# Performance work log

Measured on AMD Instinct MI355X. Metric: run time of the kernel, lower is better.

## Reference

```python
import jax, jax.numpy as jnp
import numpy as np

D_MODEL = 2048
NUM_HEADS = 16
D_FF = 8192
EPS = 1e-5


def setup_inputs() -> dict:
    key = jax.random.key(0)
    ks = jax.random.split(key, 9)
    s = 0.02
    return {
        "x": jax.random.normal(ks[0], (2, 2048, D_MODEL), dtype=jnp.float32),
        "wq": jax.random.normal(ks[1], (D_MODEL, D_MODEL), dtype=jnp.float32) * s,
        "wk": jax.random.normal(ks[2], (D_MODEL, D_MODEL), dtype=jnp.float32) * s,
        "wv": jax.random.normal(ks[3], (D_MODEL, D_MODEL), dtype=jnp.float32) * s,
        "wo": jax.random.normal(ks[4], (D_MODEL, D_MODEL), dtype=jnp.float32) * s,
        "w1": jax.random.normal(ks[5], (D_FF, D_MODEL), dtype=jnp.float32) * s,
        "w2": jax.random.normal(ks[6], (D_MODEL, D_FF), dtype=jnp.float32) * s,
        "g1": jnp.ones((D_MODEL,), dtype=jnp.float32),
        "g2": jnp.ones((D_MODEL,), dtype=jnp.float32),
    }


def rmsnorm(a, g):
    rms = jnp.sqrt(jnp.sum(a * a, axis=-1, keepdims=True) / a.shape[-1] + EPS)
    return a / rms * g


def attention(xn, wq, wk, wv, wo):
    B, S, D = xn.shape
    H, dk = NUM_HEADS, D // NUM_HEADS
    # Linear weights are (out, in); y = x @ W^T
    q = (xn @ wq.T).reshape(B, S, H, dk).transpose(0, 2, 1, 3)  # bhsd
    k = (xn @ wk.T).reshape(B, S, H, dk).transpose(0, 2, 1, 3)
    v = (xn @ wv.T).reshape(B, S, H, dk).transpose(0, 2, 1, 3)
    scores = jnp.einsum("bhqd,bhkd->bhqk", q, k) * (dk ** -0.5)
    causal = jnp.triu(jnp.ones((S, S), dtype=bool), k=1)
    scores = jnp.where(causal, -jnp.inf, scores)
    probs = jax.nn.softmax(scores, axis=-1)
    out = jnp.einsum("bhqk,bhkd->bhqd", probs, v)
    out = out.transpose(0, 2, 1, 3).reshape(B, S, D)
    return out @ wo.T


def reference(x, wq, wk, wv, wo, w1, w2, g1, g2):
    x = x + attention(rmsnorm(x, g1), wq, wk, wv, wo)
    h = jax.nn.gelu(rmsnorm(x, g2) @ w1.T, approximate=False)
    x = x + h @ w2.T
    return x
```

## Files before the change

### kernel.cpp

```cpp
#include <hip/hip_runtime.h>
#include <hip/hip_bf16.h>
#include <math.h>

#define D_MODEL 2048
#define SEQ     2048
#define BATCH   2
#define NHEAD   16
#define DK      128
#define DFF     8192
#define MROWS   (BATCH*SEQ)

typedef short short8 __attribute__((ext_vector_type(8)));
typedef float f32x4  __attribute__((ext_vector_type(4)));

__device__ __forceinline__ short f2bf(float f) {
  union { __hip_bfloat16 b; short s; } u;
  u.b = __float2bfloat16(f);
  return u.s;
}

__device__ __forceinline__ void gload_lds16(const void* g, void* l) {
  __builtin_amdgcn_global_load_lds(
      (const __attribute__((address_space(1))) unsigned int*)g,
      (__attribute__((address_space(3))) unsigned int*)l, 16, 0, 0);
}

__global__ __launch_bounds__(256) void rmsnorm_k(const float* __restrict__ x,
                                                 const float* __restrict__ g,
                                                 short* __restrict__ o) {
  const int row = blockIdx.x;
  const int t = threadIdx.x;
  const float4* xr = (const float4*)(x + (size_t)row * D_MODEL);
  const float4* gr = (const float4*)g;
  float4 v0 = xr[2*t], v1 = xr[2*t+1];
  float s = v0.x*v0.x + v0.y*v0.y + v0.z*v0.z + v0.w*v0.w
          + v1.x*v1.x + v1.y*v1.y + v1.z*v1.z + v1.w*v1.w;
  #pragma unroll
  for (int off = 1; off < 64; off <<= 1) s += __shfl_xor(s, off);
  __shared__ float red[4];
  if ((t & 63) == 0) red[t >> 6] = s;
  __syncthreads();
  float tot = red[0] + red[1] + red[2] + red[3];
  float inv = rsqrtf(tot * (1.0f / D_MODEL) + 1e-5f);
  float4 g0 = gr[2*t], g1v = gr[2*t+1];
  short8 ov;
  ov[0] = f2bf(v0.x * inv * g0.x);
  ov[1] = f2bf(v0.y * inv * g0.y);
  ov[2] = f2bf(v0.z * inv * g0.z);
  ov[3] = f2bf(v0.w * inv * g0.w);
  ov[4] = f2bf(v1.x * inv * g1v.x);
  ov[5] = f2bf(v1.y * inv * g1v.y);
  ov[6] = f2bf(v1.z * inv * g1v.z);
  ov[7] = f2bf(v1.w * inv * g1v.w);
  *((short8*)(o + (size_t)row * D_MODEL) + t) = ov;
}

__global__ __launch_bounds__(256) void f2b_k(const float* __restrict__ src,
                                             short* __restrict__ dst, int n8) {
  int i = blockIdx.x * 256 + threadIdx.x;
  if (i >= n8) return;
  const float4* s4 = (const float4*)src + 2 * (size_t)i;
  float4 a = s4[0], b = s4[1];
  short8 o = { f2bf(a.x), f2bf(a.y), f2bf(a.z), f2bf(a.w),
               f2bf(b.x), f2bf(b.y), f2bf(b.z), f2bf(b.w) };
  *((short8*)dst + i) = o;
}

template<int EPI>
__global__ __launch_bounds__(256) void gemm_fast(const short* __restrict__ A,
                                                 const short* __restrict__ B,
                                                 void* Cv,
                                                 const float* __restrict__ resid,
                                                 int M, int N, int K) {
  __shared__ __align__(16) short As[128 * 64];
  __shared__ __align__(16) short Bs[128 * 64];
  const int t = threadIdx.x;
  const int m0 = blockIdx.x * 128, n0 = blockIdx.y * 128;
  const int wave = t >> 6, lane = t & 63, lr = lane & 15, lg = lane >> 4;
  const int wr = (wave >> 1) * 64, wc = (wave & 1) * 64;

  f32x4 acc[4][4];
  const f32x4 z4 = {0.f, 0.f, 0.f, 0.f};
  #pragma unroll
  for (int m = 0; m < 4; ++m)
    #pragma unroll
    for (int n = 0; n < 4; ++n) acc[m][n] = z4;

  const int srow = t >> 3;
  const int scol = (t & 7) * 8;

  for (int k0 = 0; k0 < K; k0 += 64) {
    #pragma unroll
    for (int i = 0; i < 4; ++i) {
      int r = srow + 32 * i;
      gload_lds16(A + (size_t)(m0 + r) * K + k0 + scol, &As[r * 64 + scol]);
      gload_lds16(B + (size_t)(n0 + r) * K + k0 + scol, &Bs[r * 64 + scol]);
    }
    __syncthreads();
    #pragma unroll
    for (int kk = 0; kk < 64; kk += 32) {
      short8 af[4], bfr[4];
      #pragma unroll
      for (int m = 0; m < 4; ++m) af[m]  = *(const short8*)&As[(wr + m*16 + lr) * 64 + kk + lg*8];
      #pragma unroll
      for (int n = 0; n < 4; ++n) bfr[n] = *(const short8*)&Bs[(wc + n*16 + lr) * 64 + kk + lg*8];
      #pragma unroll
      for (int m = 0; m < 4; ++m)
        #pragma unroll
        for (int n = 0; n < 4; ++n)
          acc[m][n] = __builtin_amdgcn_mfma_f32_16x16x32_bf16(af[m], bfr[n], acc[m][n], 0, 0, 0);
    }
    __syncthreads();
  }

  #pragma unroll
  for (int m = 0; m < 4; ++m)
    #pragma unroll
    for (int n = 0; n < 4; ++n)
      #pragma unroll
      for (int r = 0; r < 4; ++r) {
        int row = m0 + wr + m*16 + lg*4 + r;
        int col = n0 + wc + n*16 + lr;
        size_t idx = (size_t)row * N + col;
        float vv = acc[m][n][r];
        if (EPI == 0) {
          ((short*)Cv)[idx] = f2bf(vv);
        } else if (EPI == 1) {
          float gl = 0.5f * vv * (1.0f + erff(vv * 0.70710678118654752f));
          ((short*)Cv)[idx] = f2bf(gl);
        } else {
          ((float*)Cv)[idx] = vv + resid[idx];
        }
      }
}

__global__ __launch_bounds__(256) void vtrans(const short* __restrict__ QKV,
                                              short* __restrict__ VT) {
  const int st = blockIdx.x;
  const int bh = blockIdx.y;
  const int b = bh >> 4, h = bh & 15;
  const int t = threadIdx.x;
  __shared__ __align__(16) short T[64 * 128];
  const short* Vsrc = QKV + ((size_t)b * SEQ) * 6144 + 2 * D_MODEL + h * DK;
  {
    int r = t >> 4, c = (t & 15) * 8;
    #pragma unroll
    for (int i = 0; i < 4; ++i) {
      int rr = r + 16 * i;
      uint4 vv = *(const uint4*)(Vsrc + (size_t)(st * 64 + rr) * 6144 + c);
      *(uint4*)&T[rr * 128 + (c ^ (((rr >> 3) & 7) << 3))] = vv;
    }
  }
  __syncthreads();
  short* dst = VT + ((size_t)bh * DK) * SEQ + st * 64;
  {
    int c2 = (t & 7) * 8;
    #pragma unroll
    for (int i = 0; i < 4; ++i) {
      int d = (t >> 3) + 32 * i;
      short8 ov;
      #pragma unroll
      for (int j = 0; j < 8; ++j)
        ov[j] = T[(c2 + j) * 128 + (d ^ ((((c2 + j) >> 3) & 7) << 3))];
      *(short8*)(dst + (size_t)d * SEQ + c2) = ov;
    }
  }
}

__global__ __launch_bounds__(512, 2) void attn3(const short* __restrict__ QKV,
                                                const short* __restrict__ VT,
                                                short* __restrict__ O) {
  const float SC = 0.12751743f;
  const int a = blockIdx.x, bh = blockIdx.y;
  const int b = bh >> 4, h = bh & 15;
  const int t = threadIdx.x, w = t >> 6, lane = t & 63, lr = lane & 15, lg = lane >> 4;
  const short* Qp = QKV + ((size_t)b * SEQ) * 6144 + h * DK;
  const short* Kp = Qp + D_MODEL;
  const short* Vp = VT + ((size_t)bh * DK) * SEQ;
  __shared__ __align__(16) short Ks[2][64 * 128];
  __shared__ __align__(16) short Vs[2][128 * 64];
  __shared__ __align__(16) short Ps[8][16][72];

  const int krr = t >> 4, kcc = (t & 15) * 8;
  const int vdd = t >> 3, vcc = (t & 7) * 8;
  const f32x4 z4 = {0.f, 0.f, 0.f, 0.f};

  for (int sub = 0; sub < 2; ++sub) {
    const int ts = sub ? (15 - a) : a;
    const int nt = 2 * ts + 2;
    const int qrow0 = ts * 128 + w * 16;

    short8 qf[4];
    #pragma unroll
    for (int ki = 0; ki < 4; ++ki)
      qf[ki] = *(const short8*)(Qp + (size_t)(qrow0 + lr) * 6144 + ki * 32 + lg * 8);

    f32x4 acc[8];
    #pragma unroll
    for (int nd = 0; nd < 8; ++nd) acc[nd] = z4;
    float mrow[4], lsum[4];
    #pragma unroll
    for (int r = 0; r < 4; ++r) { mrow[r] = -INFINITY; lsum[r] = 0.f; }

    uint4 krg[2], vrg[2];
    #pragma unroll
    for (int i = 0; i < 2; ++i) {
      krg[i] = *(const uint4*)(Kp + (size_t)(krr + 32 * i) * 6144 + kcc);
      vrg[i] = *(const uint4*)(Vp + (size_t)(vdd + 64 * i) * SEQ + vcc);
    }
    __syncthreads();
    #pragma unroll
    for (int i = 0; i < 2; ++i) {
      int r = krr + 32 * i;
      *(uint4*)&Ks[0][(r * 128 + kcc) ^ ((r & 7) << 3)] = krg[i];
      int d = vdd + 64 * i;
      *(uint4*)&Vs[0][(d * 64 + vcc) ^ ((d & 7) << 3)] = vrg[i];
    }
    __syncthreads();

    int cur = 0;
    for (int tt = 0; tt < nt; ++tt) {
      const bool pre = (tt + 1 < nt);
      if (pre) {
        #pragma unroll
        for (int i = 0; i < 2; ++i) {
          krg[i] = *(const uint4*)(Kp + (size_t)((tt + 1) * 64 + krr + 32 * i) * 6144 + kcc);
          vrg[i] = *(const uint4*)(Vp + (size_t)(vdd + 64 * i) * SEQ + (tt + 1) * 64 + vcc);
        }
      }

      f32x4 sf[4] = {z4, z4, z4, z4};
      #pragma unroll
      for (int ki = 0; ki < 4; ++ki) {
        #pragma unroll
        for (int nk = 0; nk < 4; ++nk) {
          int rr = nk * 16 + lr;
          short8 kf = *(const short8*)&Ks[cur][(rr * 128 + ki * 32 + lg * 8) ^ ((rr & 7) << 3)];
          sf[nk] = __builtin_amdgcn_mfma_f32_16x16x32_bf16(qf[ki], kf, sf[nk], 0, 0, 0);
        }
      }

      const bool diag = (tt * 64 + 63 > qrow0);
      #pragma unroll
      for (int r = 0; r < 4; ++r) {
        int qg = qrow0 + lg * 4 + r;
        float s0 = sf[0][r] * SC, s1 = sf[1][r] * SC, s2 = sf[2][r] * SC, s3 = sf[3][r] * SC;
        if (diag) {
          int c0 = tt * 64 + lr;
          s0 = (c0      <= qg) ? s0 : -3.0e38f;
          s1 = (c0 + 16 <= qg) ? s1 : -3.0e38f;
          s2 = (c0 + 32 <= qg) ? s2 : -3.0e38f;
          s3 = (c0 + 48 <= qg) ? s3 : -3.0e38f;
        }
        float mx = fmaxf(fmaxf(s0, s1), fmaxf(s2, s3));
        mx = fmaxf(mx, __shfl_xor(mx, 1));
        mx = fmaxf(mx, __shfl_xor(mx, 2));
        mx = fmaxf(mx, __shfl_xor(mx, 4));
        mx = fmaxf(mx, __shfl_xor(mx, 8));
        float mnew = fmaxf(mrow[r], mx);
        float alpha = exp2f(mrow[r] - mnew);
        mrow[r] = mnew;
        float p0 = exp2f(s0 - mnew), p1 = exp2f(s1 - mnew),
              p2 = exp2f(s2 - mnew), p3 = exp2f(s3 - mnew);
        lsum[r] = lsum[r] * alpha + ((p0 + p1) + (p2 + p3));
        #pragma unroll
        for (int nd = 0; nd < 8; ++nd) acc[nd][r] *= alpha;
        short* pr = &Ps[w][lg * 4 + r][0];
        pr[lr]      = f2bf(p0);
        pr[16 + lr] = f2bf(p1);
        pr[32 + lr] = f2bf(p2);
        pr[48 + lr] = f2bf(p3);
      }
      asm volatile("s_waitcnt lgkmcnt(0)" ::: "memory");
      __builtin_amdgcn_sched_barrier(0);

      short8 pf0 = *(const short8*)&Ps[w][lr][lg * 8];
      short8 pf1 = *(const short8*)&Ps[w][lr][32 + lg * 8];
      #pragma unroll
      for (int nd = 0; nd < 8; ++nd) {
        int rr = nd * 16 + lr;
        short8 vf0 = *(const short8*)&Vs[cur][(rr * 64 + lg * 8) ^ ((rr & 7) << 3)];
        short8 vf1 = *(const short8*)&Vs[cur][(rr * 64 + 32 + lg * 8) ^ ((rr & 7) << 3)];
        acc[nd] = __builtin_amdgcn_mfma_f32_16x16x32_bf16(pf0, vf0, acc[nd], 0, 0, 0);
        acc[nd] = __builtin_amdgcn_mfma_f32_16x16x32_bf16(pf1, vf1, acc[nd], 0, 0, 0);
      }
      __syncthreads();
      if (pre) {
        #pragma unroll
        for (int i = 0; i < 2; ++i) {
          int r = krr + 32 * i;
          *(uint4*)&Ks[cur ^ 1][(r * 128 + kcc) ^ ((r & 7) << 3)] = krg[i];
          int d = vdd + 64 * i;
          *(uint4*)&Vs[cur ^ 1][(d * 64 + vcc) ^ ((d & 7) << 3)] = vrg[i];
        }
      }
      __syncthreads();
      cur ^= 1;
    }

    float inv[4];
    #pragma unroll
    for (int r = 0; r < 4; ++r) {
      float ls = lsum[r];
      ls += __shfl_xor(ls, 1);
      ls += __shfl_xor(ls, 2);
      ls += __shfl_xor(ls, 4);
      ls += __shfl_xor(ls, 8);
      inv[r] = 1.0f / ls;
    }
    #pragma unroll
    for (int nd = 0; nd < 8; ++nd)
      #pragma unroll
      for (int r = 0; r < 4; ++r) {
        int row = qrow0 + lg * 4 + r;
        O[(size_t)(b * SEQ + row) * D_MODEL + h * DK + nd * 16 + lr] = f2bf(acc[nd][r] * inv[r]);
      }
  }
}

template<int EPI>
__global__ __launch_bounds__(256) void gemm_bt(const short* __restrict__ A,
                                               const float* __restrict__ B,
                                               void* Cv,
                                               const float* resid,
                                               int M, int N, int K) {
  __shared__ __align__(16) short As[128][72];
  __shared__ __align__(16) short Bs[128][72];
  const int t = threadIdx.x;
  const int m0 = blockIdx.x * 128, n0 = blockIdx.y * 128;
  const int wave = t >> 6, lane = t & 63, lr = lane & 15, lg = lane >> 4;
  const int wr = (wave >> 1) * 64, wc = (wave & 1) * 64;

  f32x4 acc[4][4];
  const f32x4 z4 = {0.f, 0.f, 0.f, 0.f};
  #pragma unroll
  for (int m = 0; m < 4; ++m)
    #pragma unroll
    for (int n = 0; n < 4; ++n) acc[m][n] = z4;

  int ar[4], ac[4];
  #pragma unroll
  for (int i = 0; i < 4; ++i) { int u = t + 256*i; ar[i] = u >> 3; ac[i] = (u & 7) * 8; }

  for (int k0 = 0; k0 < K; k0 += 64) {
    #pragma unroll
    for (int i = 0; i < 4; ++i) {
      uint4 va = *(const uint4*)(A + (size_t)(m0 + ar[i]) * K + k0 + ac[i]);
      *(uint4*)&As[ar[i]][ac[i]] = va;
    }
    #pragma unroll
    for (int i = 0; i < 4; ++i) {
      const float4* bp = (const float4*)(B + (size_t)(n0 + ar[i]) * K + k0 + ac[i]);
      float4 b0 = bp[0], b1 = bp[1];
      short8 pb = { f2bf(b0.x), f2bf(b0.y), f2bf(b0.z), f2bf(b0.w),
                    f2bf(b1.x), f2bf(b1.y), f2bf(b1.z), f2bf(b1.w) };
      *(short8*)&Bs[ar[i]][ac[i]] = pb;
    }
    __syncthreads();
    #pragma unroll
    for (int kk = 0; kk < 64; kk += 32) {
      short8 af[4], bfr[4];
      #pragma unroll
      for (int m = 0; m < 4; ++m) af[m]  = *(const short8*)&As[wr + m*16 + lr][kk + lg*8];
      #pragma unroll
      for (int n = 0; n < 4; ++n) bfr[n] = *(const short8*)&Bs[wc + n*16 + lr][kk + lg*8];
      #pragma unroll
      for (int m = 0; m < 4; ++m)
        #pragma unroll
        for (int n = 0; n < 4; ++n)
          acc[m][n] = __builtin_amdgcn_mfma_f32_16x16x32_bf16(af[m], bfr[n], acc[m][n], 0, 0, 0);
    }
    __syncthreads();
  }

  #pragma unroll
  for (int m = 0; m < 4; ++m)
    #pragma unroll
    for (int n = 0; n < 4; ++n)
      #pragma unroll
      for (int r = 0; r < 4; ++r) {
        int row = m0 + wr + m*16 + lg*4 + r;
        int col = n0 + wc + n*16 + lr;
        size_t idx = (size_t)row * N + col;
        float vv = acc[m][n][r];
        if (EPI == 0) {
          ((short*)Cv)[idx] = f2bf(vv);
        } else if (EPI == 1) {
          float gl = 0.5f * vv * (1.0f + erff(vv * 0.70710678118654752f));
          ((short*)Cv)[idx] = f2bf(gl);
        } else {
          ((float*)Cv)[idx] = vv + resid[idx];
        }
      }
}

__global__ __launch_bounds__(256) void attn_k(const short* __restrict__ Q,
                                              const short* __restrict__ K,
                                              const short* __restrict__ V,
                                              short* __restrict__ O) {
  const float scale = 0.08838834764831845f;
  const int qt = blockIdx.x;
  const int bh = blockIdx.y;
  const int b = bh >> 4, h = bh & 15;
  const size_t base = ((size_t)b * SEQ) * D_MODEL + (size_t)h * DK;
  const int t = threadIdx.x, wave = t >> 6, lane = t & 63, lr = lane & 15, lg = lane >> 4;

  __shared__ __align__(16) short Ks[32][136];
  __shared__ __align__(16) short Vt[128][40];
  __shared__ __align__(16) short Ps[4][32][40];

  const int qrow0 = qt * 128 + wave * 32;
  short8 qf[2][4];
  #pragma unroll
  for (int mq = 0; mq < 2; ++mq)
    #pragma unroll
    for (int ki = 0; ki < 4; ++ki)
      qf[mq][ki] = *(const short8*)(Q + base + (size_t)(qrow0 + mq*16 + lr) * D_MODEL + ki*32 + lg*8);

  f32x4 acc[2][8];
  const f32x4 z4 = {0.f, 0.f, 0.f, 0.f};
  #pragma unroll
  for (int mq = 0; mq < 2; ++mq)
    #pragma unroll
    for (int nd = 0; nd < 8; ++nd) acc[mq][nd] = z4;
  float mrow[2][4], lsum[2][4];
  #pragma unroll
  for (int mq = 0; mq < 2; ++mq)
    #pragma unroll
    for (int r = 0; r < 4; ++r) { mrow[mq][r] = -INFINITY; lsum[mq][r] = 0.f; }

  const int lastt = qt * 4 + 3;
  for (int tt = 0; tt <= lastt; ++tt) {
    #pragma unroll
    for (int i = 0; i < 2; ++i) {
      int u = t + 256*i; int r = u >> 4; int c = (u & 15) * 8;
      *(uint4*)&Ks[r][c] = *(const uint4*)(K + base + (size_t)(tt*32 + r) * D_MODEL + c);
      uint4 vv = *(const uint4*)(V + base + (size_t)(tt*32 + r) * D_MODEL + c);
      const short* sv = (const short*)&vv;
      #pragma unroll
      for (int j = 0; j < 8; ++j) Vt[c + j][r] = sv[j];
    }
    __syncthreads();
    if (tt <= qt * 4 + wave) {
      f32x4 sf[2][2] = {{z4, z4}, {z4, z4}};
      #pragma unroll
      for (int ki = 0; ki < 4; ++ki) {
        short8 kf0 = *(const short8*)&Ks[lr][ki*32 + lg*8];
        short8 kf1 = *(const short8*)&Ks[16 + lr][ki*32 + lg*8];
        sf[0][0] = __builtin_amdgcn_mfma_f32_16x16x32_bf16(qf[0][ki], kf0, sf[0][0], 0, 0, 0);
        sf[0][1] = __builtin_amdgcn_mfma_f32_16x16x32_bf16(qf[0][ki], kf1, sf[0][1], 0, 0, 0);
        sf[1][0] = __builtin_amdgcn_mfma_f32_16x16x32_bf16(qf[1][ki], kf0, sf[1][0], 0, 0, 0);
        sf[1][1] = __builtin_amdgcn_mfma_f32_16x16x32_bf16(qf[1][ki], kf1, sf[1][1], 0, 0, 0);
      }
      #pragma unroll
      for (int mq = 0; mq < 2; ++mq) {
        #pragma unroll
        for (int r = 0; r < 4; ++r) {
          int qg = qrow0 + mq*16 + lg*4 + r;
          float s0 = sf[mq][0][r] * scale;
          float s1 = sf[mq][1][r] * scale;
          if (tt*32 + lr > qg)       s0 = -INFINITY;
          if (tt*32 + 16 + lr > qg)  s1 = -INFINITY;
          float mx = fmaxf(s0, s1);
          mx = fmaxf(mx, __shfl_xor(mx, 1));
          mx = fmaxf(mx, __shfl_xor(mx, 2));
          mx = fmaxf(mx, __shfl_xor(mx, 4));
          mx = fmaxf(mx, __shfl_xor(mx, 8));
          float mnew = fmaxf(mrow[mq][r], mx);
          float alpha = __expf(mrow[mq][r] - mnew);
          mrow[mq][r] = mnew;
          float p0 = __expf(s0 - mnew);
          float p1 = __expf(s1 - mnew);
          float ps = p0 + p1;
          ps += __shfl_xor(ps, 1);
          ps += __shfl_xor(ps, 2);
          ps += __shfl_xor(ps, 4);
          ps += __shfl_xor(ps, 8);
          lsum[mq][r] = lsum[mq][r] * alpha + ps;
          #pragma unroll
          for (int nd = 0; nd < 8; ++nd) acc[mq][nd][r] *= alpha;
          Ps[wave][mq*16 + lg*4 + r][lr]      = f2bf(p0);
          Ps[wave][mq*16 + lg*4 + r][16 + lr] = f2bf(p1);
        }
      }
      asm volatile("s_waitcnt lgkmcnt(0)" ::: "memory");
      short8 pf0 = *(const short8*)&Ps[wave][lr][lg*8];
      short8 pf1 = *(const short8*)&Ps[wave][16 + lr][lg*8];
      #pragma unroll
      for (int nd = 0; nd < 8; ++nd) {
        short8 vf = *(const short8*)&Vt[nd*16 + lr][lg*8];
        acc[0][nd] = __builtin_amdgcn_mfma_f32_16x16x32_bf16(pf0, vf, acc[0][nd], 0, 0, 0);
        acc[1][nd] = __builtin_amdgcn_mfma_f32_16x16x32_bf16(pf1, vf, acc[1][nd], 0, 0, 0);
      }
    }
    __syncthreads();
  }

  #pragma unroll
  for (int mq = 0; mq < 2; ++mq)
    #pragma unroll
    for (int nd = 0; nd < 8; ++nd)
      #pragma unroll
      for (int r = 0; r < 4; ++r) {
        int row = qrow0 + mq*16 + lg*4 + r;
        O[base + (size_t)row * D_MODEL + nd*16 + lr] = f2bf(acc[mq][nd][r] / lsum[mq][r]);
      }
}

extern "C" void kernel_launch(void* const* d_in, const int* in_sizes, int n_in,
                              void* d_out, int out_size, void* d_ws, size_t ws_size,
                              hipStream_t stream) {
  const float* x  = (const float*)d_in[0];
  const float* wq = (const float*)d_in[1];
  const float* wk = (const float*)d_in[2];
  const float* wv = (const float*)d_in[3];
  const float* wo = (const float*)d_in[4];
  const float* w1 = (const float*)d_in[5];
  const float* w2 = (const float*)d_in[6];
  const float* g1 = (const float*)d_in[7];
  const float* g2 = (const float*)d_in[8];
  float* out = (float*)d_out;
  char* ws = (char*)d_ws;

  const size_t NEED = (size_t)192 << 20;
  if (ws_size >= NEED) {
    short* wqkv = (short*)(ws);
    short* wo_b = (short*)(ws + ((size_t)24 << 20));
    short* w1_b = (short*)(ws + ((size_t)32 << 20));
    short* w2_b = (short*)(ws + ((size_t)64 << 20));
    short* qkv  = (short*)(ws + ((size_t)96 << 20));
    short* vt   = (short*)(ws + ((size_t)144 << 20));
    short* ab   = (short*)(ws + ((size_t)160 << 20));
    short* xn   = (short*)(ws + ((size_t)176 << 20));
    short* hb   = (short*)(ws + ((size_t)96 << 20));

    const int NW = D_MODEL * D_MODEL / 8;
    f2b_k<<<(NW + 255) / 256, 256, 0, stream>>>(wq, wqkv,                   NW);
    f2b_k<<<(NW + 255) / 256, 256, 0, stream>>>(wk, wqkv + (size_t)D_MODEL * D_MODEL,     NW);
    f2b_k<<<(NW + 255) / 256, 256, 0, stream>>>(wv, wqkv + (size_t)2 * D_MODEL * D_MODEL, NW);
    f2b_k<<<(NW + 255) / 256, 256, 0, stream>>>(wo, wo_b, NW);
    const int NF = DFF * D_MODEL / 8;
    f2b_k<<<(NF + 255) / 256, 256, 0, stream>>>(w1, w1_b, NF);
    f2b_k<<<(NF + 255) / 256, 256, 0, stream>>>(w2, w2_b, NF);

    rmsnorm_k<<<MROWS, 256, 0, stream>>>(x, g1, xn);
    gemm_fast<0><<<dim3(MROWS/128, 6144/128), 256, 0, stream>>>(xn, wqkv, qkv, nullptr, MROWS, 6144, D_MODEL);
    vtrans<<<dim3(SEQ/64, BATCH*NHEAD), 256, 0, stream>>>(qkv, vt);
    attn3<<<dim3(8, BATCH*NHEAD), 512, 0, stream>>>(qkv, vt, ab);
    gemm_fast<2><<<dim3(MROWS/128, D_MODEL/128), 256, 0, stream>>>(ab, wo_b, out, x, MROWS, D_MODEL, D_MODEL);
    rmsnorm_k<<<MROWS, 256, 0, stream>>>(out, g2, xn);
    gemm_fast<1><<<dim3(MROWS/128, DFF/128), 256, 0, stream>>>(xn, w1_b, hb, nullptr, MROWS, DFF, D_MODEL);
    gemm_fast<2><<<dim3(MROWS/128, D_MODEL/128), 256, 0, stream>>>(hb, w2_b, out, out, MROWS, D_MODEL, DFF);
  } else {
    short* qb = (short*)(ws + ((size_t)0  << 20));
    short* kb = (short*)(ws + ((size_t)16 << 20));
    short* vb = (short*)(ws + ((size_t)32 << 20));
    short* ab = (short*)(ws + ((size_t)48 << 20));
    short* xn = (short*)(ws + ((size_t)64 << 20));
    short* hb = (short*)(ws + ((size_t)0  << 20));

    dim3 gproj(MROWS / 128, D_MODEL / 128);
    rmsnorm_k<<<MROWS, 256, 0, stream>>>(x, g1, xn);
    gemm_bt<0><<<gproj, 256, 0, stream>>>(xn, wq, qb, nullptr, MROWS, D_MODEL, D_MODEL);
    gemm_bt<0><<<gproj, 256, 0, stream>>>(xn, wk, kb, nullptr, MROWS, D_MODEL, D_MODEL);
    gemm_bt<0><<<gproj, 256, 0, stream>>>(xn, wv, vb, nullptr, MROWS, D_MODEL, D_MODEL);
    attn_k<<<dim3(SEQ / 128, BATCH * NHEAD), 256, 0, stream>>>(qb, kb, vb, ab);
    gemm_bt<2><<<gproj, 256, 0, stream>>>(ab, wo, out, x, MROWS, D_MODEL, D_MODEL);
    rmsnorm_k<<<MROWS, 256, 0, stream>>>(out, g2, xn);
    for (int half = 0; half < 2; ++half) {
      const short* xh = xn  + (size_t)half * 2048 * D_MODEL;
      float*       oh = out + (size_t)half * 2048 * D_MODEL;
      gemm_bt<1><<<dim3(2048 / 128, DFF / 128), 256, 0, stream>>>(xh, w1, hb, nullptr, 2048, DFF, D_MODEL);
      gemm_bt<2><<<dim3(2048 / 128, D_MODEL / 128), 256, 0, stream>>>(hb, w2, oh, oh, 2048, D_MODEL, DFF);
    }
  }
}
```

Baseline: 917.1 us.

## Replace GEMM with double-buffered 8-wave 128x256 tile kernel and XCD-aware block mapping

```diff
diff --git a/kernel.cpp b/kernel.cpp
--- a/kernel.cpp
+++ b/kernel.cpp
@@ -24,6 +24,8 @@
       (const __attribute__((address_space(1))) unsigned int*)g,
       (__attribute__((address_space(3))) unsigned int*)l, 16, 0, 0);
 }
+
+#define MF(a, b, c) __builtin_amdgcn_mfma_f32_16x16x32_bf16(a, b, c, 0, 0, 0)
 
 __global__ __launch_bounds__(256) void rmsnorm_k(const float* __restrict__ x,
                                                  const float* __restrict__ g,
@@ -67,17 +69,42 @@
 }
 
 template<int EPI>
-__global__ __launch_bounds__(256) void gemm_fast(const short* __restrict__ A,
+__global__ __launch_bounds__(512, 2) void gemm8p(const short* __restrict__ A,
                                                  const short* __restrict__ B,
                                                  void* Cv,
                                                  const float* __restrict__ resid,
-                                                 int M, int N, int K) {
-  __shared__ __align__(16) short As[128 * 64];
-  __shared__ __align__(16) short Bs[128 * 64];
-  const int t = threadIdx.x;
-  const int m0 = blockIdx.x * 128, n0 = blockIdx.y * 128;
-  const int wave = t >> 6, lane = t & 63, lr = lane & 15, lg = lane >> 4;
-  const int wr = (wave >> 1) * 64, wc = (wave & 1) * 64;
+                                                 int M, int N, int K, int nbx) {
+  __shared__ __align__(16) short As[2][128 * 64];
+  __shared__ __align__(16) short Bs[2][256 * 64];
+  const int nk = K >> 6;
+  const int cpx = gridDim.x >> 3;
+  const int lin = (blockIdx.x & 7) * cpx + (blockIdx.x >> 3);
+  const int bx = lin % nbx, by = lin / nbx;
+  const int m0 = bx * 128, n0 = by * 256;
+  const int t = threadIdx.x, w = t >> 6, lane = t & 63, lr = lane & 15, lg = lane >> 4;
+  const int wrA = (w >> 2) * 64, wcB = (w & 3) * 64;
+  const unsigned aBase = (unsigned)(size_t)(const __attribute__((address_space(3))) short*)&As[0][0];
+  const unsigned bBase = (unsigned)(size_t)(const __attribute__((address_space(3))) short*)&Bs[0][0];
+
+#define STG(gptr, ldsbyte) { \
+    unsigned _m0v = (unsigned)__builtin_amdgcn_readfirstlane((int)(ldsbyte)); \
+    asm volatile("s_mov_b32 m0, %1\n\tglobal_load_lds_dwordx4 %0, off" \
+                 :: "v"(gptr), "s"(_m0v) : "memory"); }
+#define STAGE_A(h, tt, pb) { \
+    int rl_ = t >> 3, cc_ = t & 7; \
+    const short* g_ = A + (size_t)(m0 + (h)*64 + rl_) * K + (tt)*64 + ((cc_ ^ (rl_ & 7)) << 3); \
+    STG(g_, aBase + (unsigned)(pb)*16384u + (unsigned)(h)*8192u + (unsigned)(w * 1024)); }
+#define STAGE_B(h, tt, pb) { \
+    { int ci_ = t;       int rl_ = ci_ >> 3, cc_ = ci_ & 7; \
+      const short* g_ = B + (size_t)(n0 + (h)*128 + rl_) * K + (tt)*64 + ((cc_ ^ (rl_ & 7)) << 3); \
+      STG(g_, bBase + (unsigned)(pb)*32768u + (unsigned)(h)*16384u + (unsigned)(w * 1024)); } \
+    { int ci_ = t + 512; int rl_ = ci_ >> 3, cc_ = ci_ & 7; \
+      const short* g_ = B + (size_t)(n0 + (h)*128 + rl_) * K + (tt)*64 + ((cc_ ^ (rl_ & 7)) << 3); \
+      STG(g_, bBase + (unsigned)(pb)*32768u + (unsigned)(h)*16384u + (unsigned)(w * 1024 + 8192)); } }
+#define RDA(dst, m_, kk_, p_) { int rr_ = wrA + (m_)*16 + lr; \
+    dst = *(const short8*)&As[p_][rr_ * 64 + (((kk_)*32 + lg*8) ^ ((rr_ & 7) << 3))]; }
+#define RDB(dst, n_, kk_, p_) { int rr_ = wcB + (n_)*16 + lr; \
+    dst = *(const short8*)&Bs[p_][rr_ * 64 + (((kk_)*32 + lg*8) ^ ((rr_ & 7) << 3))]; }
 
   f32x4 acc[4][4];
   const f32x4 z4 = {0.f, 0.f, 0.f, 0.f};
@@ -86,31 +113,58 @@
     #pragma unroll
     for (int n = 0; n < 4; ++n) acc[m][n] = z4;
 
-  const int srow = t >> 3;
-  const int scol = (t & 7) * 8;
-
-  for (int k0 = 0; k0 < K; k0 += 64) {
-    #pragma unroll
-    for (int i = 0; i < 4; ++i) {
-      int r = srow + 32 * i;
-      gload_lds16(A + (size_t)(m0 + r) * K + k0 + scol, &As[r * 64 + scol]);
-      gload_lds16(B + (size_t)(n0 + r) * K + k0 + scol, &Bs[r * 64 + scol]);
-    }
-    __syncthreads();
-    #pragma unroll
-    for (int kk = 0; kk < 64; kk += 32) {
-      short8 af[4], bfr[4];
-      #pragma unroll
-      for (int m = 0; m < 4; ++m) af[m]  = *(const short8*)&As[(wr + m*16 + lr) * 64 + kk + lg*8];
-      #pragma unroll
-      for (int n = 0; n < 4; ++n) bfr[n] = *(const short8*)&Bs[(wc + n*16 + lr) * 64 + kk + lg*8];
-      #pragma unroll
-      for (int m = 0; m < 4; ++m)
-        #pragma unroll
-        for (int n = 0; n < 4; ++n)
-          acc[m][n] = __builtin_amdgcn_mfma_f32_16x16x32_bf16(af[m], bfr[n], acc[m][n], 0, 0, 0);
-    }
-    __syncthreads();
+  STAGE_A(0, 0, 0); STAGE_A(1, 0, 0);
+  STAGE_B(0, 0, 0); STAGE_B(1, 0, 0);
+  STAGE_A(0, 1, 1); STAGE_A(1, 1, 1);
+
+  for (int tt = 0; tt < nk; ++tt) {
+    const int p = tt & 1;
+    if (tt + 1 < nk) { asm volatile("s_waitcnt vmcnt(2)" ::: "memory"); }
+    else             { asm volatile("s_waitcnt vmcnt(0)" ::: "memory"); }
+    __builtin_amdgcn_s_barrier();
+    asm volatile("" ::: "memory");
+
+    if (tt + 1 < nk) STAGE_B(0, tt + 1, p ^ 1);
+    short8 a0[4][2], b0[2][2];
+    #pragma unroll
+    for (int m = 0; m < 4; ++m) { RDA(a0[m][0], m, 0, p); RDA(a0[m][1], m, 1, p); }
+    #pragma unroll
+    for (int n = 0; n < 2; ++n) { RDB(b0[n][0], n, 0, p); RDB(b0[n][1], n, 1, p); }
+    asm volatile("" ::: "memory");
+    __builtin_amdgcn_s_barrier();
+    asm volatile("s_waitcnt lgkmcnt(0)" ::: "memory");
+    __builtin_amdgcn_sched_barrier(0);
+    __builtin_amdgcn_s_setprio(1);
+    #pragma unroll
+    for (int m = 0; m < 4; ++m)
+      #pragma unroll
+      for (int n = 0; n < 2; ++n) {
+        acc[m][n] = MF(a0[m][0], b0[n][0], acc[m][n]);
+        acc[m][n] = MF(a0[m][1], b0[n][1], acc[m][n]);
+      }
+    __builtin_amdgcn_s_setprio(0);
+    asm volatile("" ::: "memory");
+    __builtin_amdgcn_s_barrier();
+
+    if (tt + 1 < nk) STAGE_B(1, tt + 1, p ^ 1);
+    if (tt + 2 < nk) { STAGE_A(0, tt + 2, p); STAGE_A(1, tt + 2, p); }
+    short8 b1[2][2];
+    #pragma unroll
+    for (int n = 0; n < 2; ++n) { RDB(b1[n][0], n + 2, 0, p); RDB(b1[n][1], n + 2, 1, p); }
+    asm volatile("" ::: "memory");
+    __builtin_amdgcn_s_barrier();
+    asm volatile("s_waitcnt lgkmcnt(0)" ::: "memory");
+    __builtin_amdgcn_sched_barrier(0);
+    __builtin_amdgcn_s_setprio(1);
+    #pragma unroll
+    for (int m = 0; m < 4; ++m)
+      #pragma unroll
+      for (int n = 0; n < 2; ++n) {
+        acc[m][n + 2] = MF(a0[m][0], b1[n][0], acc[m][n + 2]);
+        acc[m][n + 2] = MF(a0[m][1], b1[n][1], acc[m][n + 2]);
+      }
+    __builtin_amdgcn_s_setprio(0);
+    asm volatile("" ::: "memory");
   }
 
   #pragma unroll
@@ -119,8 +173,8 @@
     for (int n = 0; n < 4; ++n)
       #pragma unroll
       for (int r = 0; r < 4; ++r) {
-        int row = m0 + wr + m*16 + lg*4 + r;
-        int col = n0 + wc + n*16 + lr;
+        int row = m0 + wrA + m * 16 + lg * 4 + r;
+        int col = n0 + wcB + n * 16 + lr;
         size_t idx = (size_t)row * N + col;
         float vv = acc[m][n][r];
         if (EPI == 0) {
@@ -132,6 +186,11 @@
           ((float*)Cv)[idx] = vv + resid[idx];
         }
       }
+#undef STG
+#undef STAGE_A
+#undef STAGE_B
+#undef RDA
+#undef RDB
 }
 
 __global__ __launch_bounds__(256) void vtrans(const short* __restrict__ QKV,
@@ -236,7 +295,7 @@
         for (int nk = 0; nk < 4; ++nk) {
           int rr = nk * 16 + lr;
           short8 kf = *(const short8*)&Ks[cur][(rr * 128 + ki * 32 + lg * 8) ^ ((rr & 7) << 3)];
-          sf[nk] = __builtin_amdgcn_mfma_f32_16x16x32_bf16(qf[ki], kf, sf[nk], 0, 0, 0);
+          sf[nk] = MF(qf[ki], kf, sf[nk]);
         }
       }
 
@@ -281,8 +340,8 @@
         int rr = nd * 16 + lr;
         short8 vf0 = *(const short8*)&Vs[cur][(rr * 64 + lg * 8) ^ ((rr & 7) << 3)];
         short8 vf1 = *(const short8*)&Vs[cur][(rr * 64 + 32 + lg * 8) ^ ((rr & 7) << 3)];
-        acc[nd] = __builtin_amdgcn_mfma_f32_16x16x32_bf16(pf0, vf0, acc[nd], 0, 0, 0);
-        acc[nd] = __builtin_amdgcn_mfma_f32_16x16x32_bf16(pf1, vf1, acc[nd], 0, 0, 0);
+        acc[nd] = MF(pf0, vf0, acc[nd]);
+        acc[nd] = MF(pf1, vf1, acc[nd]);
       }
       __syncthreads();
       if (pre) {
@@ -368,7 +427,7 @@
       for (int m = 0; m < 4; ++m)
         #pragma unroll
         for (int n = 0; n < 4; ++n)
-          acc[m][n] = __builtin_amdgcn_mfma_f32_16x16x32_bf16(af[m], bfr[n], acc[m][n], 0, 0, 0);
+          acc[m][n] = MF(af[m], bfr[n], acc[m][n]);
     }
     __syncthreads();
   }
@@ -447,10 +506,10 @@
       for (int ki = 0; ki < 4; ++ki) {
         short8 kf0 = *(const short8*)&Ks[lr][ki*32 + lg*8];
         short8 kf1 = *(const short8*)&Ks[16 + lr][ki*32 + lg*8];
-        sf[0][0] = __builtin_amdgcn_mfma_f32_16x16x32_bf16(qf[0][ki], kf0, sf[0][0], 0, 0, 0);
-        sf[0][1] = __builtin_amdgcn_mfma_f32_16x16x32_bf16(qf[0][ki], kf1, sf[0][1], 0, 0, 0);
-        sf[1][0] = __builtin_amdgcn_mfma_f32_16x16x32_bf16(qf[1][ki], kf0, sf[1][0], 0, 0, 0);
-        sf[1][1] = __builtin_amdgcn_mfma_f32_16x16x32_bf16(qf[1][ki], kf1, sf[1][1], 0, 0, 0);
+        sf[0][0] = MF(qf[0][ki], kf0, sf[0][0]);
+        sf[0][1] = MF(qf[0][ki], kf1, sf[0][1]);
+        sf[1][0] = MF(qf[1][ki], kf0, sf[1][0]);
+        sf[1][1] = MF(qf[1][ki], kf1, sf[1][1]);
       }
       #pragma unroll
       for (int mq = 0; mq < 2; ++mq) {
@@ -489,8 +548,8 @@
       #pragma unroll
       for (int nd = 0; nd < 8; ++nd) {
         short8 vf = *(const short8*)&Vt[nd*16 + lr][lg*8];
-        acc[0][nd] = __builtin_amdgcn_mfma_f32_16x16x32_bf16(pf0, vf, acc[0][nd], 0, 0, 0);
-        acc[1][nd] = __builtin_amdgcn_mfma_f32_16x16x32_bf16(pf1, vf, acc[1][nd], 0, 0, 0);
+        acc[0][nd] = MF(pf0, vf, acc[0][nd]);
+        acc[1][nd] = MF(pf1, vf, acc[1][nd]);
       }
     }
     __syncthreads();
@@ -544,13 +603,13 @@
     f2b_k<<<(NF + 255) / 256, 256, 0, stream>>>(w2, w2_b, NF);
 
     rmsnorm_k<<<MROWS, 256, 0, stream>>>(x, g1, xn);
-    gemm_fast<0><<<dim3(MROWS/128, 6144/128), 256, 0, stream>>>(xn, wqkv, qkv, nullptr, MROWS, 6144, D_MODEL);
+    gemm8p<0><<<dim3(32 * 24), 512, 0, stream>>>(xn, wqkv, qkv, nullptr, MROWS, 6144, D_MODEL, 32);
     vtrans<<<dim3(SEQ/64, BATCH*NHEAD), 256, 0, stream>>>(qkv, vt);
     attn3<<<dim3(8, BATCH*NHEAD), 512, 0, stream>>>(qkv, vt, ab);
-    gemm_fast<2><<<dim3(MROWS/128, D_MODEL/128), 256, 0, stream>>>(ab, wo_b, out, x, MROWS, D_MODEL, D_MODEL);
+    gemm8p<2><<<dim3(32 * 8), 512, 0, stream>>>(ab, wo_b, out, x, MROWS, D_MODEL, D_MODEL, 32);
     rmsnorm_k<<<MROWS, 256, 0, stream>>>(out, g2, xn);
-    gemm_fast<1><<<dim3(MROWS/128, DFF/128), 256, 0, stream>>>(xn, w1_b, hb, nullptr, MROWS, DFF, D_MODEL);
-    gemm_fast<2><<<dim3(MROWS/128, D_MODEL/128), 256, 0, stream>>>(hb, w2_b, out, out, MROWS, D_MODEL, DFF);
+    gemm8p<1><<<dim3(32 * 32), 512, 0, stream>>>(xn, w1_b, hb, nullptr, MROWS, DFF, D_MODEL, 32);
+    gemm8p<2><<<dim3(32 * 8), 512, 0, stream>>>(hb, w2_b, out, out, MROWS, D_MODEL, DFF, 32);
   } else {
     short* qb = (short*)(ws + ((size_t)0  << 20));
     short* kb = (short*)(ws + ((size_t)16 << 20));
```

Result: faster. 794.1 us (-13.4%).

## Replace 128x128 GEMM with 256x256 double-buffered swizzled GEMM and split-K FFN down projection

Applied to the files above, without the earlier changes.

```diff
diff --git a/kernel.cpp b/kernel.cpp
--- a/kernel.cpp
+++ b/kernel.cpp
@@ -19,11 +19,13 @@
   return u.s;
 }
 
-__device__ __forceinline__ void gload_lds16(const void* g, void* l) {
-  __builtin_amdgcn_global_load_lds(
-      (const __attribute__((address_space(1))) unsigned int*)g,
-      (__attribute__((address_space(3))) unsigned int*)l, 16, 0, 0);
-}
+#define MF(a, b, c) __builtin_amdgcn_mfma_f32_16x16x32_bf16(a, b, c, 0, 0, 0)
+#define BAR()   asm volatile("s_barrier" ::: "memory")
+#define LGKM0() { asm volatile("s_waitcnt lgkmcnt(0)" ::: "memory"); __builtin_amdgcn_sched_barrier(0); }
+#define STG(gptr, ldsbyte) { \
+    unsigned _m0v = (unsigned)__builtin_amdgcn_readfirstlane((int)(ldsbyte)); \
+    asm volatile("s_mov_b32 m0, %1\n\tglobal_load_lds_dwordx4 %0, off" \
+                 :: "v"(gptr), "s"(_m0v) : "memory"); }
 
 __global__ __launch_bounds__(256) void rmsnorm_k(const float* __restrict__ x,
                                                  const float* __restrict__ g,
@@ -66,70 +68,180 @@
   *((short8*)dst + i) = o;
 }
 
-template<int EPI>
-__global__ __launch_bounds__(256) void gemm_fast(const short* __restrict__ A,
-                                                 const short* __restrict__ B,
-                                                 void* Cv,
-                                                 const float* __restrict__ resid,
-                                                 int M, int N, int K) {
-  __shared__ __align__(16) short As[128 * 64];
-  __shared__ __align__(16) short Bs[128 * 64];
-  const int t = threadIdx.x;
-  const int m0 = blockIdx.x * 128, n0 = blockIdx.y * 128;
-  const int wave = t >> 6, lane = t & 63, lr = lane & 15, lg = lane >> 4;
-  const int wr = (wave >> 1) * 64, wc = (wave & 1) * 64;
-
-  f32x4 acc[4][4];
+__global__ __launch_bounds__(256) void combine_k(const float* p0, const float* p1,
+                                                 const float* r, float* o, int n4) {
+  int i = blockIdx.x * 256 + threadIdx.x;
+  if (i >= n4) return;
+  const float4 a = ((const float4*)p0)[i];
+  const float4 b = ((const float4*)p1)[i];
+  const float4 c = ((const float4*)r)[i];
+  float4 d;
+  d.x = a.x + b.x + c.x; d.y = a.y + b.y + c.y;
+  d.z = a.z + b.z + c.z; d.w = a.w + b.w + c.w;
+  ((float4*)o)[i] = d;
+}
+
+template<int EPI, int SPLIT>
+__global__ __launch_bounds__(512, 2) void gemm256(const short* __restrict__ A,
+                                                  const short* __restrict__ Bp,
+                                                  void* Cv,
+                                                  const float* __restrict__ resid,
+                                                  int M, int N, int K,
+                                                  int lda, int ldb, int nbx) {
+  __shared__ __align__(16) short As[2][2][128 * 64];
+  __shared__ __align__(16) short Bs[2][2][128 * 64];
+  const int nk = K >> 6;
+  const int cpx = gridDim.x >> 3;
+  const int lin = (blockIdx.x & 7) * cpx + (blockIdx.x >> 3);
+  const int bx = lin % nbx;
+  int row2 = lin / nbx, by, ks = 0;
+  if (SPLIT) { ks = row2 & 1; by = row2 >> 1; } else { by = row2; }
+  const int m0 = bx * 256, n0 = by * 256;
+  if (SPLIT) { A += (size_t)ks * K; Bp += (size_t)ks * K; }
+
+  const int t = threadIdx.x, w = t >> 6, lane = t & 63, lr = lane & 15, lg = lane >> 4;
+  const int wm = w >> 2, wn = w & 3;
+  const unsigned aByte = (unsigned)(size_t)(const __attribute__((address_space(3))) short*)&As[0][0][0];
+  const unsigned bByte = (unsigned)(size_t)(const __attribute__((address_space(3))) short*)&Bs[0][0][0];
+  const unsigned wOff = (unsigned)(w * 1024);
+
+  const int r = t >> 3, c8 = t & 7;
+  const int sw = (c8 ^ (r & 7)) << 3;
+  const short* pA0 = A  + (size_t)(m0 + r)       * lda + sw;
+  const short* pA1 = A  + (size_t)(m0 + 128 + r) * lda + sw;
+  const short* pB0 = Bp + (size_t)(n0 + r)       * ldb + sw;
+  const short* pB1 = Bp + (size_t)(n0 + 128 + r) * ldb + sw;
+  const size_t l64A = (size_t)64 * lda, l64B = (size_t)64 * ldb;
+
+  f32x4 acc[8][4];
   const f32x4 z4 = {0.f, 0.f, 0.f, 0.f};
   #pragma unroll
-  for (int m = 0; m < 4; ++m)
+  for (int m = 0; m < 8; ++m)
     #pragma unroll
     for (int n = 0; n < 4; ++n) acc[m][n] = z4;
 
-  const int srow = t >> 3;
-  const int scol = (t & 7) * 8;
-
-  for (int k0 = 0; k0 < K; k0 += 64) {
-    #pragma unroll
-    for (int i = 0; i < 4; ++i) {
-      int r = srow + 32 * i;
-      gload_lds16(A + (size_t)(m0 + r) * K + k0 + scol, &As[r * 64 + scol]);
-      gload_lds16(B + (size_t)(n0 + r) * K + k0 + scol, &Bs[r * 64 + scol]);
-    }
-    __syncthreads();
-    #pragma unroll
-    for (int kk = 0; kk < 64; kk += 32) {
-      short8 af[4], bfr[4];
-      #pragma unroll
-      for (int m = 0; m < 4; ++m) af[m]  = *(const short8*)&As[(wr + m*16 + lr) * 64 + kk + lg*8];
-      #pragma unroll
-      for (int n = 0; n < 4; ++n) bfr[n] = *(const short8*)&Bs[(wc + n*16 + lr) * 64 + kk + lg*8];
-      #pragma unroll
-      for (int m = 0; m < 4; ++m)
-        #pragma unroll
-        for (int n = 0; n < 4; ++n)
-          acc[m][n] = __builtin_amdgcn_mfma_f32_16x16x32_bf16(af[m], bfr[n], acc[m][n], 0, 0, 0);
-    }
-    __syncthreads();
-  }
-
-  #pragma unroll
-  for (int m = 0; m < 4; ++m)
+  STG(pA0,        aByte + wOff);                 STG(pA0 + l64A,      aByte + 8192 + wOff);
+  STG(pA1,        aByte + 16384 + wOff);         STG(pA1 + l64A,      aByte + 16384 + 8192 + wOff);
+  STG(pB0,        bByte + wOff);                 STG(pB0 + l64B,      bByte + 8192 + wOff);
+  STG(pB1,        bByte + 16384 + wOff);         STG(pB1 + l64B,      bByte + 16384 + 8192 + wOff);
+  if (nk > 1) {
+    STG(pB0 + 64, bByte + 32768 + wOff);         STG(pB0 + 64 + l64B, bByte + 32768 + 8192 + wOff);
+    STG(pB1 + 64, bByte + 32768 + 16384 + wOff); STG(pB1 + 64 + l64B, bByte + 32768 + 16384 + 8192 + wOff);
+    STG(pA0 + 64, aByte + 32768 + wOff);         STG(pA0 + 64 + l64A, aByte + 32768 + 8192 + wOff);
+    asm volatile("s_waitcnt vmcnt(6)" ::: "memory");
+  } else {
+    asm volatile("s_waitcnt vmcnt(0)" ::: "memory");
+  }
+  BAR();
+
+  for (int T = 0; T < nk; ++T) {
+    const int p = T & 1, q = p ^ 1;
+    const unsigned aS = aByte + (unsigned)p * 32768u, aQ = aByte + (unsigned)q * 32768u;
+    const unsigned bS = bByte + (unsigned)p * 32768u;
+
+    if (T + 1 < nk) {
+      const short* s = pA1 + (size_t)(T + 1) * 64;
+      STG(s, aQ + 16384u + wOff); STG(s + l64A, aQ + 16384u + 8192u + wOff);
+    }
+    short8 bk0[4], bk1[4], aA[4];
+    #pragma unroll
+    for (int n = 0; n < 4; ++n) {
+      int br = wn * 64 + n * 16 + lr;
+      const short* bp = &Bs[p][br >> 7][(br & 127) * 64];
+      bk0[n] = *(const short8*)&bp[(lg * 8)      ^ ((br & 7) << 3)];
+      bk1[n] = *(const short8*)&bp[(32 + lg * 8) ^ ((br & 7) << 3)];
+    }
+    #pragma unroll
+    for (int m = 0; m < 4; ++m) {
+      int ar = m * 16 + lr;
+      aA[m] = *(const short8*)&As[p][wm][ar * 64 + ((lg * 8) ^ ((ar & 7) << 3))];
+    }
+    BAR(); LGKM0();
+    __builtin_amdgcn_s_setprio(1);
+    #pragma unroll
+    for (int m = 0; m < 4; ++m)
+      #pragma unroll
+      for (int n = 0; n < 4; ++n) acc[m][n] = MF(aA[m], bk0[n], acc[m][n]);
+    __builtin_amdgcn_s_setprio(0);
+    BAR();
+
+    if (T + 2 < nk) {
+      const short* s = pB0 + (size_t)(T + 2) * 64;
+      STG(s, bS + wOff); STG(s + l64B, bS + 8192u + wOff);
+    }
+    short8 aB[4], aC[4];
+    #pragma unroll
+    for (int m = 0; m < 4; ++m) {
+      int ar = 64 + m * 16 + lr;
+      aB[m] = *(const short8*)&As[p][wm][ar * 64 + ((lg * 8) ^ ((ar & 7) << 3))];
+      int ar2 = m * 16 + lr;
+      aC[m] = *(const short8*)&As[p][wm][ar2 * 64 + ((32 + lg * 8) ^ ((ar2 & 7) << 3))];
+    }
+    BAR(); LGKM0();
+    __builtin_amdgcn_s_setprio(1);
+    #pragma unroll
+    for (int m = 0; m < 4; ++m)
+      #pragma unroll
+      for (int n = 0; n < 4; ++n) acc[m + 4][n] = MF(aB[m], bk0[n], acc[m + 4][n]);
+    __builtin_amdgcn_s_setprio(0);
+    BAR();
+
+    if (T + 2 < nk) {
+      const short* s = pB1 + (size_t)(T + 2) * 64;
+      STG(s, bS + 16384u + wOff); STG(s + l64B, bS + 16384u + 8192u + wOff);
+    }
+    short8 aD[4];
+    #pragma unroll
+    for (int m = 0; m < 4; ++m) {
+      int ar = 64 + m * 16 + lr;
+      aD[m] = *(const short8*)&As[p][wm][ar * 64 + ((32 + lg * 8) ^ ((ar & 7) << 3))];
+    }
+    BAR(); LGKM0();
+    __builtin_amdgcn_s_setprio(1);
+    #pragma unroll
+    for (int m = 0; m < 4; ++m)
+      #pragma unroll
+      for (int n = 0; n < 4; ++n) acc[m][n] = MF(aC[m], bk1[n], acc[m][n]);
+    __builtin_amdgcn_s_setprio(0);
+    BAR();
+
+    if (T + 2 < nk) {
+      const short* s = pA0 + (size_t)(T + 2) * 64;
+      STG(s, aS + wOff); STG(s + l64A, aS + 8192u + wOff);
+    }
+    BAR(); LGKM0();
+    __builtin_amdgcn_s_setprio(1);
+    #pragma unroll
+    for (int m = 0; m < 4; ++m)
+      #pragma unroll
+      for (int n = 0; n < 4; ++n) acc[m + 4][n] = MF(aD[m], bk1[n], acc[m + 4][n]);
+    __builtin_amdgcn_s_setprio(0);
+
+    if (T + 2 < nk)      { asm volatile("s_waitcnt vmcnt(6)" ::: "memory"); BAR(); }
+    else if (T + 1 < nk) { asm volatile("s_waitcnt vmcnt(0)" ::: "memory"); BAR(); }
+  }
+
+  float* Cf = (float*)Cv;
+  if (SPLIT) Cf += (size_t)ks * ((size_t)M * N);
+  #pragma unroll
+  for (int m = 0; m < 8; ++m)
     #pragma unroll
     for (int n = 0; n < 4; ++n)
       #pragma unroll
-      for (int r = 0; r < 4; ++r) {
-        int row = m0 + wr + m*16 + lg*4 + r;
-        int col = n0 + wc + n*16 + lr;
+      for (int rr = 0; rr < 4; ++rr) {
+        int row = m0 + wm * 128 + m * 16 + lg * 4 + rr;
+        int col = n0 + wn * 64 + n * 16 + lr;
         size_t idx = (size_t)row * N + col;
-        float vv = acc[m][n][r];
+        float vv = acc[m][n][rr];
         if (EPI == 0) {
           ((short*)Cv)[idx] = f2bf(vv);
         } else if (EPI == 1) {
           float gl = 0.5f * vv * (1.0f + erff(vv * 0.70710678118654752f));
           ((short*)Cv)[idx] = f2bf(gl);
+        } else if (EPI == 2) {
+          ((float*)Cv)[idx] = vv + resid[idx];
         } else {
-          ((float*)Cv)[idx] = vv + resid[idx];
+          Cf[idx] = vv;
         }
       }
 }
@@ -236,7 +348,7 @@
         for (int nk = 0; nk < 4; ++nk) {
           int rr = nk * 16 + lr;
           short8 kf = *(const short8*)&Ks[cur][(rr * 128 + ki * 32 + lg * 8) ^ ((rr & 7) << 3)];
-          sf[nk] = __builtin_amdgcn_mfma_f32_16x16x32_bf16(qf[ki], kf, sf[nk], 0, 0, 0);
+          sf[nk] = MF(qf[ki], kf, sf[nk]);
         }
       }
 
@@ -281,8 +393,8 @@
         int rr = nd * 16 + lr;
         short8 vf0 = *(const short8*)&Vs[cur][(rr * 64 + lg * 8) ^ ((rr & 7) << 3)];
         short8 vf1 = *(const short8*)&Vs[cur][(rr * 64 + 32 + lg * 8) ^ ((rr & 7) << 3)];
-        acc[nd] = __builtin_amdgcn_mfma_f32_16x16x32_bf16(pf0, vf0, acc[nd], 0, 0, 0);
-        acc[nd] = __builtin_amdgcn_mfma_f32_16x16x32_bf16(pf1, vf1, acc[nd], 0, 0, 0);
+        acc[nd] = MF(pf0, vf0, acc[nd]);
+        acc[nd] = MF(pf1, vf1, acc[nd]);
       }
       __syncthreads();
       if (pre) {
@@ -368,7 +480,7 @@
       for (int m = 0; m < 4; ++m)
         #pragma unroll
         for (int n = 0; n < 4; ++n)
-          acc[m][n] = __builtin_amdgcn_mfma_f32_16x16x32_bf16(af[m], bfr[n], acc[m][n], 0, 0, 0);
+          acc[m][n] = MF(af[m], bfr[n], acc[m][n]);
     }
     __syncthreads();
   }
@@ -447,10 +559,10 @@
       for (int ki = 0; ki < 4; ++ki) {
         short8 kf0 = *(const short8*)&Ks[lr][ki*32 + lg*8];
         short8 kf1 = *(const short8*)&Ks[16 + lr][ki*32 + lg*8];
-        sf[0][0] = __builtin_amdgcn_mfma_f32_16x16x32_bf16(qf[0][ki], kf0, sf[0][0], 0, 0, 0);
-        sf[0][1] = __builtin_amdgcn_mfma_f32_16x16x32_bf16(qf[0][ki], kf1, sf[0][1], 0, 0, 0);
-        sf[1][0] = __builtin_amdgcn_mfma_f32_16x16x32_bf16(qf[1][ki], kf0, sf[1][0], 0, 0, 0);
-        sf[1][1] = __builtin_amdgcn_mfma_f32_16x16x32_bf16(qf[1][ki], kf1, sf[1][1], 0, 0, 0);
+        sf[0][0] = MF(qf[0][ki], kf0, sf[0][0]);
+        sf[0][1] = MF(qf[0][ki], kf1, sf[0][1]);
+        sf[1][0] = MF(qf[1][ki], kf0, sf[1][0]);
+        sf[1][1] = MF(qf[1][ki], kf1, sf[1][1]);
       }
       #pragma unroll
       for (int mq = 0; mq < 2; ++mq) {
@@ -489,8 +601,8 @@
       #pragma unroll
       for (int nd = 0; nd < 8; ++nd) {
         short8 vf = *(const short8*)&Vt[nd*16 + lr][lg*8];
-        acc[0][nd] = __builtin_amdgcn_mfma_f32_16x16x32_bf16(pf0, vf, acc[0][nd], 0, 0, 0);
-        acc[1][nd] = __builtin_amdgcn_mfma_f32_16x16x32_bf16(pf1, vf, acc[1][nd], 0, 0, 0);
+        acc[0][nd] = MF(pf0, vf, acc[0][nd]);
+        acc[1][nd] = MF(pf1, vf, acc[1][nd]);
       }
     }
     __syncthreads();
@@ -533,6 +645,7 @@
     short* ab   = (short*)(ws + ((size_t)160 << 20));
     short* xn   = (short*)(ws + ((size_t)176 << 20));
     short* hb   = (short*)(ws + ((size_t)96 << 20));
+    float* pf   = (float*)(ws + ((size_t)160 << 20));
 
     const int NW = D_MODEL * D_MODEL / 8;
     f2b_k<<<(NW + 255) / 256, 256, 0, stream>>>(wq, wqkv,                   NW);
@@ -544,13 +657,19 @@
     f2b_k<<<(NF + 255) / 256, 256, 0, stream>>>(w2, w2_b, NF);
 
     rmsnorm_k<<<MROWS, 256, 0, stream>>>(x, g1, xn);
-    gemm_fast<0><<<dim3(MROWS/128, 6144/128), 256, 0, stream>>>(xn, wqkv, qkv, nullptr, MROWS, 6144, D_MODEL);
+    gemm256<0,0><<<dim3(16 * 24), 512, 0, stream>>>(xn, wqkv, qkv, nullptr,
+                                                    MROWS, 6144, D_MODEL, D_MODEL, D_MODEL, 16);
     vtrans<<<dim3(SEQ/64, BATCH*NHEAD), 256, 0, stream>>>(qkv, vt);
     attn3<<<dim3(8, BATCH*NHEAD), 512, 0, stream>>>(qkv, vt, ab);
-    gemm_fast<2><<<dim3(MROWS/128, D_MODEL/128), 256, 0, stream>>>(ab, wo_b, out, x, MROWS, D_MODEL, D_MODEL);
+    gemm256<2,0><<<dim3(16 * 8), 512, 0, stream>>>(ab, wo_b, out, x,
+                                                   MROWS, D_MODEL, D_MODEL, D_MODEL, D_MODEL, 16);
     rmsnorm_k<<<MROWS, 256, 0, stream>>>(out, g2, xn);
-    gemm_fast<1><<<dim3(MROWS/128, DFF/128), 256, 0, stream>>>(xn, w1_b, hb, nullptr, MROWS, DFF, D_MODEL);
-    gemm_fast<2><<<dim3(MROWS/128, D_MODEL/128), 256, 0, stream>>>(hb, w2_b, out, out, MROWS, D_MODEL, DFF);
+    gemm256<1,0><<<dim3(16 * 32), 512, 0, stream>>>(xn, w1_b, hb, nullptr,
+                                                    MROWS, DFF, D_MODEL, D_MODEL, D_MODEL, 16);
+    gemm256<3,1><<<dim3(16 * 8 * 2), 512, 0, stream>>>(hb, w2_b, pf, nullptr,
+                                                       MROWS, D_MODEL, DFF / 2, DFF, DFF, 16);
+    const int N4 = MROWS * D_MODEL / 4;
+    combine_k<<<(N4 + 255) / 256, 256, 0, stream>>>(pf, pf + (size_t)MROWS * D_MODEL, out, out, N4);
   } else {
     short* qb = (short*)(ws + ((size_t)0  << 20));
     short* kb = (short*)(ws + ((size_t)16 << 20));
```

Measured after the change: 757.8 us. 17.4% less time.
